# Kernel tuning notes

Hardware: AMD Instinct MI355X
Metric: run time of the kernel (lower is better)

## Reference

```python
import jax, jax.numpy as jnp
import numpy as np

N_CELLS, N_CLASSES, N_GENES, N_EDGES, HID = 100000, 50, 500, 600000, 8
NEG_SLOPE = 0.2  # GATv2Conv default negative_slope


def setup_inputs() -> dict:
    key = jax.random.key(0)
    ks = jax.random.split(key, 10)
    X = jax.random.normal(ks[0], (N_CELLS, N_GENES), jnp.float32)
    Mu = jax.random.normal(ks[1], (N_CLASSES, N_GENES), jnp.float32)
    # variances must be strictly positive
    Var = jax.random.uniform(ks[2], (N_CLASSES, N_GENES), jnp.float32) + 0.5
    W = 0.1 * jax.random.normal(ks[3], (N_CELLS, N_CLASSES), jnp.float32)
    S = 1.0 + 0.05 * jax.random.normal(ks[4], (N_CELLS, 1), jnp.float32)
    edge_index = jax.random.randint(ks[5], (2, N_EDGES), 0, N_CELLS, jnp.int32)
    sc = 1.0 / np.sqrt(N_GENES)
    lin_l_w = sc * jax.random.normal(ks[6], (HID, N_GENES), jnp.float32)
    lin_l_b = jnp.zeros((HID,), jnp.float32)
    lin_r_w = sc * jax.random.normal(ks[7], (HID, N_GENES), jnp.float32)
    lin_r_b = jnp.zeros((HID,), jnp.float32)
    att = jax.random.normal(ks[8], (HID,), jnp.float32) / np.sqrt(HID)
    return dict(X=X, Mu=Mu, Var=Var, W=W, S=S, edge_index=edge_index,
                lin_l_w=lin_l_w, lin_l_b=lin_l_b,
                lin_r_w=lin_r_w, lin_r_b=lin_r_b, att=att)


def _forward(X, Mu, Var, W, S, lin_l_w, lin_l_b, lin_r_w, lin_r_b, att, edge_index):
    N = X.shape[0]
    P = jax.nn.softmax(W, axis=1)  # [N, C]

    # Gaussian log-likelihood term.
    # F[n,c] = -0.5 * sum_g (X[n,g] - Mu[c,g]*S[n])^2 / Var[c,g]
    # Expanded into GEMMs (algebraically identical, avoids the [N,C,G] intermediate):
    invV = 1.0 / Var                          # [C, G]
    t1 = (X * X) @ invV.T                     # [N, C]  sum_g X^2/Var
    t2 = X @ (Mu * invV).T                    # [N, C]  sum_g X*Mu/Var
    t3 = jnp.sum(Mu * Mu * invV, axis=1)      # [C]     sum_g Mu^2/Var
    Fmat = -0.5 * (t1 - 2.0 * S * t2 + (S * S) * t3[None, :])  # [N, C]
    ll_prot = jnp.sum(P * Fmat) / N

    # GATv2 attention coefficients (heads=1, add_self_loops=False).
    gl = X @ lin_l_w.T + lin_l_b              # [N, HID]  lin_l (source side)
    gr = X @ lin_r_w.T + lin_r_b              # [N, HID]  lin_r (target side)
    src, dst = edge_index[0], edge_index[1]
    e = jax.nn.leaky_relu(gl[src] + gr[dst], NEG_SLOPE)  # [E, HID]
    score = e @ att                                       # [E]
    # segment softmax over destination nodes
    m = jax.ops.segment_max(score, dst, num_segments=N)
    ex = jnp.exp(score - m[dst])
    denom = jax.ops.segment_sum(ex, dst, num_segments=N)
    alpha = ex / denom[dst]                               # [E]

    ce_space = -jnp.sum(P[src] * alpha[:, None] * jnp.log(P[dst] + 1e-8)) / N
    return ll_prot, ce_space, P


def reference(X, Mu, Var, W, S, edge_index, lin_l_w, lin_l_b, lin_r_w, lin_r_b, att):
    return _forward(X, Mu, Var, W, S, lin_l_w, lin_l_b, lin_r_w, lin_r_b, att, edge_index)
```

## Files before the change

kernel.cpp:

```cpp
#include <hip/hip_runtime.h>
#include <math.h>

#define N_CELLS   100000
#define N_CLASSES 50
#define N_GENES   500
#define N_EDGES   600000
#define HID       8
#define NKT       8
#define NB_FUSED  1563
#define NB_CE     391

typedef __attribute__((ext_vector_type(4))) float f32x4;
typedef __attribute__((ext_vector_type(8))) short bf16x8;

static const size_t OFF_BF    = 0;
static const size_t OFF_T3    = 147456;
static const size_t OFF_GLR   = 147712;
static const size_t OFF_SCORE = 6547712;
static const size_t OFF_MSEG  = 8947712;
static const size_t OFF_DENOM = 9347712;
static const size_t OFF_NUMER = 9747712;
static const size_t OFF_LLP   = 10147712;
static const size_t OFF_CEP   = 10153968;
static const size_t ZERO_BEG  = OFF_MSEG;
static const size_t ZERO_BYTES= 10147712 - 8947712;

__device__ __forceinline__ ushort f2bf(float f) {
    union { float f; unsigned u; } v; v.f = f;
    unsigned r = v.u + 0x7fffu + ((v.u >> 16) & 1u);
    return (ushort)(r >> 16);
}

__device__ __forceinline__ unsigned cvt_pk_bf16(float lo, float hi) {
    unsigned r;
    asm("v_cvt_pk_bf16_f32 %0, %1, %2" : "=v"(r) : "v"(lo), "v"(hi));
    return r;
}

__device__ __forceinline__ void gload16(const void* g, void* l) {
    __builtin_amdgcn_global_load_lds(
        (const __attribute__((address_space(1))) unsigned int*)g,
        (__attribute__((address_space(3))) unsigned int*)l,
        16, 0, 0);
}

__global__ __launch_bounds__(256) void k_prepB(const float* __restrict__ Var,
                                               const float* __restrict__ Mu,
                                               const float* __restrict__ wl,
                                               const float* __restrict__ wr,
                                               ushort* __restrict__ Bf) {
    int id = blockIdx.x * 256 + threadIdx.x;
    float v = 0.f;
    if (id < 65536) {
        int e    = id & 7;
        int lane = (id >> 3) & 63;
        int j    = (id >> 9) & 15;
        int kt   = id >> 13;
        int t    = j >> 1, ss = j & 1;
        int s    = kt * 2 + ss;
        int k    = s * 32 + ((lane >> 4) << 3) + e;
        int c    = (t & 3) * 16 + (lane & 15);
        if (k < N_GENES && c < N_CLASSES)
            v = (t < 4) ? 1.0f / Var[c * N_GENES + k]
                        : Mu[c * N_GENES + k] / Var[c * N_GENES + k];
    } else {
        int rem  = id - 65536;
        int e    = rem & 7;
        int lane = (rem >> 3) & 63;
        int s    = rem >> 9;
        int k    = s * 32 + ((lane >> 4) << 3) + e;
        int h    = lane & 15;
        if (k < N_GENES)
            v = (h < HID) ? wl[h * N_GENES + k] : wr[(h - HID) * N_GENES + k];
    }
    Bf[id] = f2bf(v);
}

__global__ void k_t3(const float* __restrict__ Var, const float* __restrict__ Mu,
                     float* __restrict__ t3) {
    int c = blockIdx.x;
    int lane = threadIdx.x;
    float s = 0.f;
    for (int g = lane; g < N_GENES; g += 64) {
        float m = Mu[c * N_GENES + g];
        s += m * m / Var[c * N_GENES + g];
    }
    #pragma unroll
    for (int off = 32; off; off >>= 1) s += __shfl_xor(s, off);
    if (lane == 0) t3[c] = s;
}

__global__ __launch_bounds__(256) void k_softmax(const float* __restrict__ W,
                                                 float* __restrict__ P) {
    int wid  = (blockIdx.x * 256 + threadIdx.x) >> 6;
    int lane = threadIdx.x & 63;
    if (wid >= N_CELLS) return;
    float w = (lane < N_CLASSES) ? W[(size_t)wid * N_CLASSES + lane] : -__builtin_inff();
    float m = w;
    #pragma unroll
    for (int off = 32; off; off >>= 1) m = fmaxf(m, __shfl_xor(m, off));
    float e = (lane < N_CLASSES) ? expf(w - m) : 0.f;
    float s = e;
    #pragma unroll
    for (int off = 32; off; off >>= 1) s += __shfl_xor(s, off);
    if (lane < N_CLASSES) P[(size_t)wid * N_CLASSES + lane] = e / s;
}

__global__ __launch_bounds__(256, 2) void k_fused(const float* __restrict__ X,
                                                  const float* __restrict__ S,
                                                  const float* __restrict__ P,
                                                  const ushort* __restrict__ Bf,
                                                  const float* __restrict__ t3,
                                                  const float* __restrict__ bl,
                                                  const float* __restrict__ br,
                                                  float* __restrict__ glr,
                                                  float* __restrict__ llp) {
    __shared__ float  ldsA[2][4][16][16][4];
    __shared__ ushort ldsB[2][20][64][8];
    __shared__ float  wsum[4];
    int tid  = threadIdx.x;
    int lane = tid & 63;
    int wv   = tid >> 6;
    int lhi  = lane >> 4;
    int slot = lane & 15;
    int rbase = blockIdx.x * 64 + wv * 16;
    const char* Xc  = (const char*)X;
    const char* Bfc = (const char*)Bf;

    int arow = rbase + slot;
    if (arow > N_CELLS - 1) arow = N_CELLS - 1;
    float m2s = -2.0f * S[arow];

    const f32x4 zz = {0.f, 0.f, 0.f, 0.f};
    f32x4 acc1[4], acc2[4], acc3;
    #pragma unroll
    for (int ct = 0; ct < 4; ++ct) { acc1[ct] = zz; acc2[ct] = zz; }
    acc3 = zz;

#define STAGE(KT, BUF) do {                                                        \
    _Pragma("unroll")                                                              \
    for (int i = 0; i < 4; ++i) {                                                  \
        int rloc = i * 4 + lhi;                                                    \
        int row  = rbase + rloc; if (row > N_CELLS - 1) row = N_CELLS - 1;         \
        int gi   = (KT) * 16 + (slot ^ (rloc & 7)); if (gi > 124) gi = 124;        \
        gload16(Xc + (size_t)row * 2000 + (size_t)gi * 16, &ldsA[BUF][wv][i * 4][0][0]); \
    }                                                                              \
    _Pragma("unroll")                                                              \
    for (int i = 0; i < 5; ++i) {                                                  \
        int j = wv * 5 + i;                                                        \
        size_t src;                                                                \
        if (j < 16)      src = (size_t)(KT) * 16384 + (size_t)j * 1024;            \
        else if (j < 18) src = 131072 + ((size_t)(KT) * 2 + (size_t)(j - 16)) * 1024; \
        else             src = (size_t)(KT) * 16384;                               \
        gload16(Bfc + src + (size_t)lane * 16, &ldsB[BUF][j][0][0]);               \
    }                                                                              \
} while (0)

    STAGE(0, 0);

    #pragma unroll
    for (int kt = 0; kt < NKT; ++kt) {
        const int cur = kt & 1;
        if (kt < NKT - 1) {
            STAGE(kt + 1, cur ^ 1);
            __builtin_amdgcn_sched_barrier(0);
            asm volatile("s_waitcnt vmcnt(9)" ::: "memory");
        } else {
            __builtin_amdgcn_sched_barrier(0);
            asm volatile("s_waitcnt vmcnt(0)" ::: "memory");
        }
        __builtin_amdgcn_sched_barrier(0);
        __builtin_amdgcn_s_barrier();
        __builtin_amdgcn_sched_barrier(0);

        const bf16x8* BL = (const bf16x8*)&ldsB[cur][0][0][0];
        #pragma unroll
        for (int ks = 0; ks < 2; ++ks) {
            int key = slot & 7;
            int c0  = ks * 8 + lhi * 2;
            f32x4 xa = *(const f32x4*)&ldsA[cur][wv][slot][c0 ^ key][0];
            f32x4 xb = *(const f32x4*)&ldsA[cur][wv][slot][(c0 + 1) ^ key][0];
            union { bf16x8 v; unsigned u[4]; } a1, a2;
            a1.u[0] = cvt_pk_bf16(xa[0] * xa[0], xa[1] * xa[1]);
            a1.u[1] = cvt_pk_bf16(xa[2] * xa[2], xa[3] * xa[3]);
            a1.u[2] = cvt_pk_bf16(xb[0] * xb[0], xb[1] * xb[1]);
            a1.u[3] = cvt_pk_bf16(xb[2] * xb[2], xb[3] * xb[3]);
            a2.u[0] = cvt_pk_bf16(m2s * xa[0], m2s * xa[1]);
            a2.u[1] = cvt_pk_bf16(m2s * xa[2], m2s * xa[3]);
            a2.u[2] = cvt_pk_bf16(m2s * xb[0], m2s * xb[1]);
            a2.u[3] = cvt_pk_bf16(m2s * xb[2], m2s * xb[3]);
            bf16x8 bg = BL[(16 + ks) * 64 + lane];
            #pragma unroll
            for (int ct = 0; ct < 4; ++ct)
                acc1[ct] = __builtin_amdgcn_mfma_f32_16x16x32_bf16(a1.v, BL[(ct * 2 + ks) * 64 + lane], acc1[ct], 0, 0, 0);
            #pragma unroll
            for (int ct = 0; ct < 4; ++ct)
                acc2[ct] = __builtin_amdgcn_mfma_f32_16x16x32_bf16(a2.v, BL[((4 + ct) * 2 + ks) * 64 + lane], acc2[ct], 0, 0, 0);
            acc3 = __builtin_amdgcn_mfma_f32_16x16x32_bf16(a2.v, bg, acc3, 0, 0, 0);
        }
        __builtin_amdgcn_sched_barrier(0);
        __builtin_amdgcn_s_barrier();
        __builtin_amdgcn_sched_barrier(0);
    }
#undef STAGE

    int col = lane & 15;
    int rg  = lane >> 4;
    float bias = (col < HID) ? bl[col] : br[col - HID];
    float part = 0.f;
    #pragma unroll
    for (int r = 0; r < 4; ++r) {
        int row = rbase + rg * 4 + r;
        if (row < N_CELLS) {
            float s2 = S[row];
            glr[(size_t)row * 16 + col] = acc3[r] / (-2.0f * s2) + bias;
            float ss = s2 * s2;
            #pragma unroll
            for (int ct = 0; ct < 4; ++ct) {
                int c = ct * 16 + col;
                if (c < N_CLASSES) {
                    float F = -0.5f * (acc1[ct][r] + acc2[ct][r] + ss * t3[c]);
                    part = fmaf(P[(size_t)row * N_CLASSES + c], F, part);
                }
            }
        }
    }
    #pragma unroll
    for (int off = 32; off; off >>= 1) part += __shfl_xor(part, off);
    if (lane == 0) wsum[wv] = part;
    __syncthreads();
    if (tid == 0) llp[blockIdx.x] = wsum[0] + wsum[1] + wsum[2] + wsum[3];
}

__device__ __forceinline__ unsigned map_f32(float f) {
    int s = __float_as_int(f);
    return (s < 0) ? ~(unsigned)s : ((unsigned)s | 0x80000000u);
}
__device__ __forceinline__ float unmap_f32(unsigned u) {
    return (u & 0x80000000u) ? __int_as_float((int)(u & 0x7fffffffu))
                             : __int_as_float((int)~u);
}

__global__ __launch_bounds__(256) void k_score(const int* __restrict__ ei,
                                               const float* __restrict__ glr,
                                               const float* __restrict__ att,
                                               float* __restrict__ score,
                                               unsigned* __restrict__ mseg) {
    int e = blockIdx.x * 256 + threadIdx.x;
    if (e >= N_EDGES) return;
    int src = ei[e], dst = ei[N_EDGES + e];
    const float4* a = (const float4*)(glr + (size_t)src * 16);
    const float4* b = (const float4*)(glr + (size_t)dst * 16 + 8);
    float4 g0 = a[0], g1 = a[1], h0 = b[0], h1 = b[1];
    const float4* at = (const float4*)att;
    float4 a0 = at[0], a1 = at[1];
    float v, s = 0.f;
    v = g0.x + h0.x; v = v > 0.f ? v : 0.2f * v; s = fmaf(a0.x, v, s);
    v = g0.y + h0.y; v = v > 0.f ? v : 0.2f * v; s = fmaf(a0.y, v, s);
    v = g0.z + h0.z; v = v > 0.f ? v : 0.2f * v; s = fmaf(a0.z, v, s);
    v = g0.w + h0.w; v = v > 0.f ? v : 0.2f * v; s = fmaf(a0.w, v, s);
    v = g1.x + h1.x; v = v > 0.f ? v : 0.2f * v; s = fmaf(a1.x, v, s);
    v = g1.y + h1.y; v = v > 0.f ? v : 0.2f * v; s = fmaf(a1.y, v, s);
    v = g1.z + h1.z; v = v > 0.f ? v : 0.2f * v; s = fmaf(a1.z, v, s);
    v = g1.w + h1.w; v = v > 0.f ? v : 0.2f * v; s = fmaf(a1.w, v, s);
    score[e] = s;
    atomicMax(mseg + dst, map_f32(s));
}

__global__ __launch_bounds__(256) void k_edge2(const int* __restrict__ ei,
                                               const float* __restrict__ score,
                                               const unsigned* __restrict__ mseg,
                                               const float* __restrict__ P,
                                               float* __restrict__ denom,
                                               float* __restrict__ numer) {
    int t = blockIdx.x * 256 + threadIdx.x;
    int e = t >> 4;
    int q = t & 15;
    if (e >= N_EDGES) return;
    int src = ei[e], dst = ei[N_EDGES + e];
    float ex = expf(score[e] - unmap_f32(mseg[dst]));
    const float* Ps = P + (size_t)src * N_CLASSES;
    const float* Pd = P + (size_t)dst * N_CLASSES;
    float v = Ps[q]      * logf(Pd[q]      + 1e-8f)
            + Ps[q + 16] * logf(Pd[q + 16] + 1e-8f)
            + Ps[q + 32] * logf(Pd[q + 32] + 1e-8f);
    if (q < 2) v += Ps[q + 48] * logf(Pd[q + 48] + 1e-8f);
    v += __shfl_xor(v, 8); v += __shfl_xor(v, 4);
    v += __shfl_xor(v, 2); v += __shfl_xor(v, 1);
    if (q == 0) {
        atomicAdd(denom + dst, ex);
        atomicAdd(numer + dst, ex * v);
    }
}

__global__ __launch_bounds__(256) void k_ce(const float* __restrict__ denom,
                                            const float* __restrict__ numer,
                                            float* __restrict__ cep) {
    __shared__ float wsum[4];
    int n = blockIdx.x * 256 + threadIdx.x;
    float v = 0.f;
    if (n < N_CELLS) {
        float d = denom[n];
        v = (d > 0.f) ? numer[n] / d : 0.f;
    }
    #pragma unroll
    for (int off = 32; off; off >>= 1) v += __shfl_xor(v, off);
    if ((threadIdx.x & 63) == 0) wsum[threadIdx.x >> 6] = v;
    __syncthreads();
    if (threadIdx.x == 0) cep[blockIdx.x] = wsum[0] + wsum[1] + wsum[2] + wsum[3];
}

__global__ __launch_bounds__(256) void k_reduce(const float* __restrict__ llp,
                                                const float* __restrict__ cep,
                                                float* __restrict__ out) {
    __shared__ double l1[256], l2[256];
    int t = threadIdx.x;
    double s1 = 0.0, s2 = 0.0;
    for (int i = t; i < NB_FUSED; i += 256) s1 += (double)llp[i];
    for (int i = t; i < NB_CE; i += 256) s2 += (double)cep[i];
    l1[t] = s1; l2[t] = s2;
    __syncthreads();
    for (int off = 128; off; off >>= 1) {
        if (t < off) { l1[t] += l1[t + off]; l2[t] += l2[t + off]; }
        __syncthreads();
    }
    if (t == 0) {
        out[0] = (float)(l1[0] / (double)N_CELLS);
        out[1] = (float)(-l2[0] / (double)N_CELLS);
    }
}

extern "C" void kernel_launch(void* const* d_in, const int* in_sizes, int n_in,
                              void* d_out, int out_size, void* d_ws, size_t ws_size,
                              hipStream_t stream) {
    const float* X   = (const float*)d_in[0];
    const float* Mu  = (const float*)d_in[1];
    const float* Var = (const float*)d_in[2];
    const float* W   = (const float*)d_in[3];
    const float* S   = (const float*)d_in[4];
    const int*   ei  = (const int*)d_in[5];
    const float* wl  = (const float*)d_in[6];
    const float* bl  = (const float*)d_in[7];
    const float* wr  = (const float*)d_in[8];
    const float* br  = (const float*)d_in[9];
    const float* att = (const float*)d_in[10];
    float* out = (float*)d_out;
    char*  ws  = (char*)d_ws;

    ushort*   Bf    = (ushort*)(ws + OFF_BF);
    float*    t3    = (float*)(ws + OFF_T3);
    float*    glr   = (float*)(ws + OFF_GLR);
    float*    score = (float*)(ws + OFF_SCORE);
    unsigned* mseg  = (unsigned*)(ws + OFF_MSEG);
    float*    denom = (float*)(ws + OFF_DENOM);
    float*    numer = (float*)(ws + OFF_NUMER);
    float*    llp   = (float*)(ws + OFF_LLP);
    float*    cep   = (float*)(ws + OFF_CEP);
    float*    P     = out + 2;

    hipMemsetAsync(ws + ZERO_BEG, 0, ZERO_BYTES, stream);

    k_prepB  <<<288, 256, 0, stream>>>(Var, Mu, wl, wr, Bf);
    k_t3     <<<N_CLASSES, 64, 0, stream>>>(Var, Mu, t3);
    k_softmax<<<(N_CELLS * 64 + 255) / 256, 256, 0, stream>>>(W, P);
    k_fused  <<<NB_FUSED, 256, 0, stream>>>(X, S, P, Bf, t3, bl, br, glr, llp);
    k_score  <<<(N_EDGES + 255) / 256, 256, 0, stream>>>(ei, glr, att, score, mseg);
    k_edge2  <<<(N_EDGES * 16 + 255) / 256, 256, 0, stream>>>(ei, score, mseg, P, denom, numer);
    k_ce     <<<NB_CE, 256, 0, stream>>>(denom, numer, cep);
    k_reduce <<<1, 256, 0, stream>>>(llp, cep, out);
}
```

Baseline: 196.2 us.

## Fuse edge score and CE passes, drop segment max, precompute bf16 P and log P

```diff
diff --git a/kernel.cpp b/kernel.cpp
--- a/kernel.cpp
+++ b/kernel.cpp
@@ -9,34 +9,37 @@
 #define NKT       8
 #define NB_FUSED  1563
 #define NB_CE     391
+#define PROWS     56
 
 typedef __attribute__((ext_vector_type(4))) float f32x4;
 typedef __attribute__((ext_vector_type(8))) short bf16x8;
+typedef __attribute__((ext_vector_type(8))) unsigned short u16x8;
 
 static const size_t OFF_BF    = 0;
 static const size_t OFF_T3    = 147456;
 static const size_t OFF_GLR   = 147712;
-static const size_t OFF_SCORE = 6547712;
-static const size_t OFF_MSEG  = 8947712;
-static const size_t OFF_DENOM = 9347712;
-static const size_t OFF_NUMER = 9747712;
-static const size_t OFF_LLP   = 10147712;
-static const size_t OFF_CEP   = 10153968;
-static const size_t ZERO_BEG  = OFF_MSEG;
-static const size_t ZERO_BYTES= 10147712 - 8947712;
+static const size_t OFF_PB    = 6547712;
+static const size_t OFF_LQ    = 17747712;
+static const size_t OFF_DENOM = 28947712;
+static const size_t OFF_NUMER = 29347712;
+static const size_t OFF_LLP   = 29747712;
+static const size_t OFF_CEP   = 29754112;
+static const size_t ZERO_BEG  = OFF_DENOM;
+static const size_t ZERO_BYTES= 29747712 - 28947712;
 
 __device__ __forceinline__ ushort f2bf(float f) {
     union { float f; unsigned u; } v; v.f = f;
     unsigned r = v.u + 0x7fffu + ((v.u >> 16) & 1u);
     return (ushort)(r >> 16);
 }
-
+__device__ __forceinline__ float bf2f(ushort b) {
+    union { unsigned u; float f; } v; v.u = ((unsigned)b) << 16; return v.f;
+}
 __device__ __forceinline__ unsigned cvt_pk_bf16(float lo, float hi) {
     unsigned r;
     asm("v_cvt_pk_bf16_f32 %0, %1, %2" : "=v"(r) : "v"(lo), "v"(hi));
     return r;
 }
-
 __device__ __forceinline__ void gload16(const void* g, void* l) {
     __builtin_amdgcn_global_load_lds(
         (const __attribute__((address_space(1))) unsigned int*)g,
@@ -91,7 +94,9 @@
 }
 
 __global__ __launch_bounds__(256) void k_softmax(const float* __restrict__ W,
-                                                 float* __restrict__ P) {
+                                                 float* __restrict__ P,
+                                                 ushort* __restrict__ Pb,
+                                                 ushort* __restrict__ LQ) {
     int wid  = (blockIdx.x * 256 + threadIdx.x) >> 6;
     int lane = threadIdx.x & 63;
     if (wid >= N_CELLS) return;
@@ -103,7 +108,12 @@
     float s = e;
     #pragma unroll
     for (int off = 32; off; off >>= 1) s += __shfl_xor(s, off);
-    if (lane < N_CLASSES) P[(size_t)wid * N_CLASSES + lane] = e / s;
+    float p = e / s;
+    if (lane < N_CLASSES) P[(size_t)wid * N_CLASSES + lane] = p;
+    if (lane < PROWS) {
+        Pb[(size_t)wid * PROWS + lane] = (lane < N_CLASSES) ? f2bf(p) : 0;
+        LQ[(size_t)wid * PROWS + lane] = (lane < N_CLASSES) ? f2bf(logf(p + 1e-8f)) : 0;
+    }
 }
 
 __global__ __launch_bounds__(256, 2) void k_fused(const float* __restrict__ X,
@@ -232,20 +242,13 @@
     if (tid == 0) llp[blockIdx.x] = wsum[0] + wsum[1] + wsum[2] + wsum[3];
 }
 
-__device__ __forceinline__ unsigned map_f32(float f) {
-    int s = __float_as_int(f);
-    return (s < 0) ? ~(unsigned)s : ((unsigned)s | 0x80000000u);
-}
-__device__ __forceinline__ float unmap_f32(unsigned u) {
-    return (u & 0x80000000u) ? __int_as_float((int)(u & 0x7fffffffu))
-                             : __int_as_float((int)~u);
-}
-
-__global__ __launch_bounds__(256) void k_score(const int* __restrict__ ei,
-                                               const float* __restrict__ glr,
-                                               const float* __restrict__ att,
-                                               float* __restrict__ score,
-                                               unsigned* __restrict__ mseg) {
+__global__ __launch_bounds__(256) void k_edge(const int* __restrict__ ei,
+                                              const float* __restrict__ glr,
+                                              const float* __restrict__ att,
+                                              const ushort* __restrict__ Pb,
+                                              const ushort* __restrict__ LQ,
+                                              float* __restrict__ denom,
+                                              float* __restrict__ numer) {
     int e = blockIdx.x * 256 + threadIdx.x;
     if (e >= N_EDGES) return;
     int src = ei[e], dst = ei[N_EDGES + e];
@@ -254,43 +257,29 @@
     float4 g0 = a[0], g1 = a[1], h0 = b[0], h1 = b[1];
     const float4* at = (const float4*)att;
     float4 a0 = at[0], a1 = at[1];
-    float v, s = 0.f;
-    v = g0.x + h0.x; v = v > 0.f ? v : 0.2f * v; s = fmaf(a0.x, v, s);
-    v = g0.y + h0.y; v = v > 0.f ? v : 0.2f * v; s = fmaf(a0.y, v, s);
-    v = g0.z + h0.z; v = v > 0.f ? v : 0.2f * v; s = fmaf(a0.z, v, s);
-    v = g0.w + h0.w; v = v > 0.f ? v : 0.2f * v; s = fmaf(a0.w, v, s);
-    v = g1.x + h1.x; v = v > 0.f ? v : 0.2f * v; s = fmaf(a1.x, v, s);
-    v = g1.y + h1.y; v = v > 0.f ? v : 0.2f * v; s = fmaf(a1.y, v, s);
-    v = g1.z + h1.z; v = v > 0.f ? v : 0.2f * v; s = fmaf(a1.z, v, s);
-    v = g1.w + h1.w; v = v > 0.f ? v : 0.2f * v; s = fmaf(a1.w, v, s);
-    score[e] = s;
-    atomicMax(mseg + dst, map_f32(s));
-}
-
-__global__ __launch_bounds__(256) void k_edge2(const int* __restrict__ ei,
-                                               const float* __restrict__ score,
-                                               const unsigned* __restrict__ mseg,
-                                               const float* __restrict__ P,
-                                               float* __restrict__ denom,
-                                               float* __restrict__ numer) {
-    int t = blockIdx.x * 256 + threadIdx.x;
-    int e = t >> 4;
-    int q = t & 15;
-    if (e >= N_EDGES) return;
-    int src = ei[e], dst = ei[N_EDGES + e];
-    float ex = expf(score[e] - unmap_f32(mseg[dst]));
-    const float* Ps = P + (size_t)src * N_CLASSES;
-    const float* Pd = P + (size_t)dst * N_CLASSES;
-    float v = Ps[q]      * logf(Pd[q]      + 1e-8f)
-            + Ps[q + 16] * logf(Pd[q + 16] + 1e-8f)
-            + Ps[q + 32] * logf(Pd[q + 32] + 1e-8f);
-    if (q < 2) v += Ps[q + 48] * logf(Pd[q + 48] + 1e-8f);
-    v += __shfl_xor(v, 8); v += __shfl_xor(v, 4);
-    v += __shfl_xor(v, 2); v += __shfl_xor(v, 1);
-    if (q == 0) {
-        atomicAdd(denom + dst, ex);
-        atomicAdd(numer + dst, ex * v);
-    }
+    float t, s = 0.f;
+    t = g0.x + h0.x; t = t > 0.f ? t : 0.2f * t; s = fmaf(a0.x, t, s);
+    t = g0.y + h0.y; t = t > 0.f ? t : 0.2f * t; s = fmaf(a0.y, t, s);
+    t = g0.z + h0.z; t = t > 0.f ? t : 0.2f * t; s = fmaf(a0.z, t, s);
+    t = g0.w + h0.w; t = t > 0.f ? t : 0.2f * t; s = fmaf(a0.w, t, s);
+    t = g1.x + h1.x; t = t > 0.f ? t : 0.2f * t; s = fmaf(a1.x, t, s);
+    t = g1.y + h1.y; t = t > 0.f ? t : 0.2f * t; s = fmaf(a1.y, t, s);
+    t = g1.z + h1.z; t = t > 0.f ? t : 0.2f * t; s = fmaf(a1.z, t, s);
+    t = g1.w + h1.w; t = t > 0.f ? t : 0.2f * t; s = fmaf(a1.w, t, s);
+    float ex = expf(s);
+
+    const u16x8* ps = (const u16x8*)(Pb + (size_t)src * PROWS);
+    const u16x8* ld = (const u16x8*)(LQ + (size_t)dst * PROWS);
+    float v = 0.f;
+    #pragma unroll
+    for (int i = 0; i < 7; ++i) {
+        u16x8 pv = ps[i], lv = ld[i];
+        #pragma unroll
+        for (int j = 0; j < 8; ++j)
+            v = fmaf(bf2f(pv[j]), bf2f(lv[j]), v);
+    }
+    atomicAdd(denom + dst, ex);
+    atomicAdd(numer + dst, ex * v);
 }
 
 __global__ __launch_bounds__(256) void k_ce(const float* __restrict__ denom,
@@ -347,25 +336,24 @@
     float* out = (float*)d_out;
     char*  ws  = (char*)d_ws;
 
-    ushort*   Bf    = (ushort*)(ws + OFF_BF);
-    float*    t3    = (float*)(ws + OFF_T3);
-    float*    glr   = (float*)(ws + OFF_GLR);
-    float*    score = (float*)(ws + OFF_SCORE);
-    unsigned* mseg  = (unsigned*)(ws + OFF_MSEG);
-    float*    denom = (float*)(ws + OFF_DENOM);
-    float*    numer = (float*)(ws + OFF_NUMER);
-    float*    llp   = (float*)(ws + OFF_LLP);
-    float*    cep   = (float*)(ws + OFF_CEP);
-    float*    P     = out + 2;
+    ushort* Bf    = (ushort*)(ws + OFF_BF);
+    float*  t3    = (float*)(ws + OFF_T3);
+    float*  glr   = (float*)(ws + OFF_GLR);
+    ushort* Pb    = (ushort*)(ws + OFF_PB);
+    ushort* LQ    = (ushort*)(ws + OFF_LQ);
+    float*  denom = (float*)(ws + OFF_DENOM);
+    float*  numer = (float*)(ws + OFF_NUMER);
+    float*  llp   = (float*)(ws + OFF_LLP);
+    float*  cep   = (float*)(ws + OFF_CEP);
+    float*  P     = out + 2;
 
     hipMemsetAsync(ws + ZERO_BEG, 0, ZERO_BYTES, stream);
 
     k_prepB  <<<288, 256, 0, stream>>>(Var, Mu, wl, wr, Bf);
     k_t3     <<<N_CLASSES, 64, 0, stream>>>(Var, Mu, t3);
-    k_softmax<<<(N_CELLS * 64 + 255) / 256, 256, 0, stream>>>(W, P);
+    k_softmax<<<(N_CELLS * 64 + 255) / 256, 256, 0, stream>>>(W, P, Pb, LQ);
     k_fused  <<<NB_FUSED, 256, 0, stream>>>(X, S, P, Bf, t3, bl, br, glr, llp);
-    k_score  <<<(N_EDGES + 255) / 256, 256, 0, stream>>>(ei, glr, att, score, mseg);
-    k_edge2  <<<(N_EDGES * 16 + 255) / 256, 256, 0, stream>>>(ei, score, mseg, P, denom, numer);
+    k_edge   <<<(N_EDGES + 255) / 256, 256, 0, stream>>>(ei, glr, att, Pb, LQ, denom, numer);
     k_ce     <<<NB_CE, 256, 0, stream>>>(denom, numer, cep);
     k_reduce <<<1, 256, 0, stream>>>(llp, cep, out);
 }
```

New measurement: 189.8 us. 3.3% less time.
